# Kernel tuning notes

Measured on AMD Instinct MI355X. Metric: run time of the kernel, lower is better.

## Reference

```python
import jax, jax.numpy as jnp
import numpy as np

B, C, H, W = 8, 64, 256, 256
K = 3  # num_experts in CondConv2D


def setup_inputs() -> dict:
    key = jax.random.key(0)
    ks = jax.random.split(key, 10)
    s = 0.05
    return {
        "x":    jax.random.normal(ks[0], (B, C, H, W), jnp.float32),
        # CondConv2D #1: depthwise 5x5, pad 2, dil 1
        "w0":   jax.random.normal(ks[1], (K, C, 1, 5, 5), jnp.float32) * s,
        "b0":   jax.random.normal(ks[2], (C,), jnp.float32) * s,
        "r0_w": jax.random.normal(ks[3], (K, C), jnp.float32) * s,
        "r0_b": jnp.zeros((K,), jnp.float32),
        # CondConv2D #2: depthwise 7x7, pad 9, dil 3
        "w1":   jax.random.normal(ks[4], (K, C, 1, 7, 7), jnp.float32) * s,
        "b1":   jax.random.normal(ks[5], (C,), jnp.float32) * s,
        "r1_w": jax.random.normal(ks[6], (K, C), jnp.float32) * s,
        "r1_b": jnp.zeros((K,), jnp.float32),
        # conv1: 1x1 pointwise
        "wp":   jax.random.normal(ks[7], (C, C), jnp.float32) * s,
        "bp":   jnp.zeros((C,), jnp.float32),
    }


def cond_dwconv(x, weight, bias, rw, rb, pad, dil):
    """Per-sample expert-mixed depthwise conv (CondConv with groups=C).
    x: [B,C,H,W]; weight: [K,C,1,ks,ks]; rw: [K,C], rb: [K]."""
    b, c, h, w = x.shape
    pooled = x.mean(axis=(2, 3))                      # [B,C] adaptive avg pool to 1x1
    r = jax.nn.sigmoid(pooled @ rw.T + rb)            # [B,K] routing weights
    wk = jnp.einsum('bk,kcihw->bcihw', r, weight)     # [B,C,1,ks,ks] mixed kernels
    ksz = weight.shape[-1]
    # batch-folded grouped conv: fold B into channel/group dim
    out = jax.lax.conv_general_dilated(
        x.reshape(1, b * c, h, w),
        wk.reshape(b * c, 1, ksz, ksz),
        window_strides=(1, 1),
        padding=[(pad, pad), (pad, pad)],
        rhs_dilation=(dil, dil),
        feature_group_count=b * c,
        dimension_numbers=('NCHW', 'OIHW', 'NCHW'))
    return out.reshape(b, c, h, w) + bias[None, :, None, None]


def reference(x, w0, b0, r0_w, r0_b, w1, b1, r1_w, r1_b, wp, bp):
    attn = jax.nn.gelu(cond_dwconv(x, w0, b0, r0_w, r0_b, pad=2, dil=1), approximate=False)
    attn = jax.nn.gelu(cond_dwconv(attn, w1, b1, r1_w, r1_b, pad=9, dil=3), approximate=False)
    attn = jnp.einsum('bchw,oc->bohw', attn, wp) + bp[None, :, None, None]  # 1x1 conv
    return x * attn
```

## Files before the change

kernel.cpp:

```cpp
#include <hip/hip_runtime.h>
#include <hip/hip_fp16.h>

#define HW 65536
#define PW 256
#define C7S 168

__device__ __forceinline__ float gelu_f(float v) {
    return 0.5f * v * (1.0f + erff(v * 0.7071067811865476f));
}

__device__ __forceinline__ unsigned pack2h(float a, float b) {
    __half2 h = __floats2half2_rn(a, b);
    return *reinterpret_cast<unsigned*>(&h);
}

__device__ __forceinline__ void unpack8(uint4 u, float* dst) {
    float2 f;
    f = __half22float2(*reinterpret_cast<__half2*>(&u.x)); dst[0] = f.x; dst[1] = f.y;
    f = __half22float2(*reinterpret_cast<__half2*>(&u.y)); dst[2] = f.x; dst[3] = f.y;
    f = __half22float2(*reinterpret_cast<__half2*>(&u.z)); dst[4] = f.x; dst[5] = f.y;
    f = __half22float2(*reinterpret_cast<__half2*>(&u.w)); dst[6] = f.x; dst[7] = f.y;
}

__device__ __forceinline__ float sgpr_f(float v) {
    union { float f; int i; } u;
    u.f = v;
    u.i = __builtin_amdgcn_readfirstlane(u.i);
    return u.f;
}

__global__ __launch_bounds__(256) void k_pool_x(const float* __restrict__ x,
                                                float* __restrict__ partial) {
    __shared__ float red[256];
    const int t = threadIdx.x;
    const int blk = blockIdx.x;
    const float* p = x + (size_t)blk * 16384;
    float s = 0.f;
    #pragma unroll
    for (int i = 0; i < 16; ++i) {
        float4 v = *reinterpret_cast<const float4*>(p + (i * 256 + t) * 4);
        s += v.x + v.y + v.z + v.w;
    }
    red[t] = s;
    __syncthreads();
    for (int off = 128; off > 0; off >>= 1) {
        if (t < off) red[t] += red[t + off];
        __syncthreads();
    }
    if (t == 0) partial[blk] = red[0];
}

__global__ __launch_bounds__(64) void k_route_mix(const float* __restrict__ partial,
                                                  const float* __restrict__ rw,
                                                  const float* __restrict__ rb,
                                                  const float* __restrict__ wexp,
                                                  float* __restrict__ wkout, int taps) {
    __shared__ float pool_s[64];
    __shared__ float r_s[3];
    const int b = blockIdx.x, c = threadIdx.x;
    float s = 0.f;
    #pragma unroll
    for (int q = 0; q < 4; ++q) s += partial[(b * 64 + c) * 4 + q];
    pool_s[c] = s * (1.0f / 65536.0f);
    __syncthreads();
    if (c < 3) {
        float z = rb[c];
        #pragma unroll
        for (int i = 0; i < 64; ++i) z += pool_s[i] * rw[c * 64 + i];
        r_s[c] = 1.0f / (1.0f + expf(-z));
    }
    __syncthreads();
    const float r0 = r_s[0], r1 = r_s[1], r2 = r_s[2];
    for (int j = 0; j < taps; ++j) {
        wkout[(b * 64 + c) * taps + j] =
            r0 * wexp[(0 * 64 + c) * taps + j] +
            r1 * wexp[(1 * 64 + c) * taps + j] +
            r2 * wexp[(2 * 64 + c) * taps + j];
    }
}

__global__ __launch_bounds__(256) void k_conv5(const float* __restrict__ x,
                                               const float* __restrict__ wk,
                                               const float* __restrict__ bias,
                                               __half* __restrict__ attn0,
                                               float* __restrict__ tilesum) {
    __shared__ float red[256];
    const int blk = blockIdx.x;
    const int plane = blk >> 2;
    const int tile = blk & 3;
    const int c = plane & 63;
    const int oy0 = (tile >> 1) << 7;
    const int ox0 = (tile & 1) << 7;
    const int t = threadIdx.x;
    const int ox = ox0 + ((t & 15) << 3);
    const int oy = oy0 + ((t >> 4) << 3);
    const float* xp = x + (size_t)plane * HW;
    const float* wkp = wk + plane * 25;
    float w[25];
    #pragma unroll
    for (int i = 0; i < 25; ++i) w[i] = sgpr_f(wkp[i]);
    float acc[8][8];
    #pragma unroll
    for (int i = 0; i < 8; ++i)
        #pragma unroll
        for (int j = 0; j < 8; ++j) acc[i][j] = 0.f;

    #pragma unroll
    for (int r = 0; r < 12; ++r) {
        const int gy = oy - 2 + r;
        if (gy >= 0 && gy < 256) {
            const float* rp = xp + gy * PW + ox;
            float buf[16];
            float4 v;
            if (ox > 0) v = *reinterpret_cast<const float4*>(rp - 4);
            else        v = make_float4(0.f, 0.f, 0.f, 0.f);
            buf[0] = v.x; buf[1] = v.y; buf[2] = v.z; buf[3] = v.w;
            v = *reinterpret_cast<const float4*>(rp);
            buf[4] = v.x; buf[5] = v.y; buf[6] = v.z; buf[7] = v.w;
            v = *reinterpret_cast<const float4*>(rp + 4);
            buf[8] = v.x; buf[9] = v.y; buf[10] = v.z; buf[11] = v.w;
            if (ox < 248) v = *reinterpret_cast<const float4*>(rp + 8);
            else          v = make_float4(0.f, 0.f, 0.f, 0.f);
            buf[12] = v.x; buf[13] = v.y; buf[14] = v.z; buf[15] = v.w;
            #pragma unroll
            for (int i = 0; i < 8; ++i) {
                const int d = r - i;
                if (d >= 0 && d <= 4) {
                    #pragma unroll
                    for (int dx = 0; dx < 5; ++dx) {
                        const float wv = w[d * 5 + dx];
                        #pragma unroll
                        for (int j = 0; j < 8; ++j)
                            acc[i][j] += wv * buf[j + dx + 2];
                    }
                }
            }
        }
    }
    const float bs = bias[c];
    float lsum = 0.f;
    __half* op = attn0 + (size_t)plane * HW;
    #pragma unroll
    for (int i = 0; i < 8; ++i) {
        float g[8];
        #pragma unroll
        for (int j = 0; j < 8; ++j) {
            g[j] = gelu_f(acc[i][j] + bs);
            lsum += g[j];
        }
        uint4 st;
        st.x = pack2h(g[0], g[1]); st.y = pack2h(g[2], g[3]);
        st.z = pack2h(g[4], g[5]); st.w = pack2h(g[6], g[7]);
        *reinterpret_cast<uint4*>(op + (oy + i) * PW + ox) = st;
    }
    red[t] = lsum;
    __syncthreads();
    for (int off = 128; off > 0; off >>= 1) {
        if (t < off) red[t] += red[t + off];
        __syncthreads();
    }
    if (t == 0) tilesum[blk] = red[0];
}

__global__ __launch_bounds__(256) void k_conv7(const __half* __restrict__ a0,
                                               const float* __restrict__ wk,
                                               const float* __restrict__ bias,
                                               __half* __restrict__ attn1) {
    __shared__ __half lds[82 * C7S];
    const int blk = blockIdx.x;
    const int plane = blk >> 3;
    const int tile = blk & 7;
    const int c = plane & 63;
    const int oy0 = (tile >> 1) << 6;
    const int ox0 = (tile & 1) << 7;
    const int t = threadIdx.x;
    const __half* ap = a0 + (size_t)plane * HW;

    const uint4 z4 = make_uint4(0u, 0u, 0u, 0u);
    #pragma unroll
    for (int it = 0; it < 7; ++it) {
        const int idx = it * 256 + t;
        if (idx < 1722) {
            const int lr = idx / 21;
            const int c8 = idx - lr * 21;
            const int gy = oy0 - 9 + lr;
            const int gx = ox0 - 16 + (c8 << 3);
            uint4 v = z4;
            if ((unsigned)gy < 256u && (unsigned)gx < 256u)
                v = *reinterpret_cast<const uint4*>(ap + gy * PW + gx);
            *reinterpret_cast<uint4*>(&lds[lr * C7S + (c8 << 3)]) = v;
        }
    }

    float w[49];
    #pragma unroll
    for (int i = 0; i < 49; ++i) w[i] = sgpr_f(wk[plane * 49 + i]);
    __syncthreads();

    const int tx = t & 3, ty = t >> 2;
    const int ox = tx << 5;
    float acc[32];
    #pragma unroll
    for (int j = 0; j < 32; ++j) acc[j] = 0.f;

    #pragma unroll
    for (int dyi = 0; dyi < 7; ++dyi) {
        const int lr = ty + 3 * dyi;
        const __half* lp = &lds[lr * C7S + ox];
        float buf[64];
        #pragma unroll
        for (int k = 0; k < 8; ++k) {
            uint4 u = *reinterpret_cast<const uint4*>(lp + (k << 3));
            unpack8(u, buf + (k << 3));
        }
        #pragma unroll
        for (int dxi = 0; dxi < 7; ++dxi) {
            const float wv = w[dyi * 7 + dxi];
            #pragma unroll
            for (int j = 0; j < 32; ++j)
                acc[j] += wv * buf[7 + j + 3 * dxi];
        }
    }

    const float bs = bias[c];
    __half* op = attn1 + (size_t)plane * HW + (size_t)(oy0 + ty) * PW + ox0 + ox;
    #pragma unroll
    for (int q = 0; q < 4; ++q) {
        float g[8];
        #pragma unroll
        for (int j = 0; j < 8; ++j) g[j] = gelu_f(acc[q * 8 + j] + bs);
        uint4 st;
        st.x = pack2h(g[0], g[1]); st.y = pack2h(g[2], g[3]);
        st.z = pack2h(g[4], g[5]); st.w = pack2h(g[6], g[7]);
        *reinterpret_cast<uint4*>(op + (q << 3)) = st;
    }
}

__global__ __launch_bounds__(256) void k_mix(const __half* __restrict__ attn1,
                                             const float* __restrict__ wpm,
                                             const float* __restrict__ bp,
                                             const float* __restrict__ x,
                                             float* __restrict__ out) {
    __shared__ __half A_s[64][256];
    __shared__ float wpT[64][64];
    const int t = threadIdx.x;
    const int blk = blockIdx.x;
    const int b = blk >> 8;
    const int p0g = (blk & 255) << 8;
    #pragma unroll
    for (int it = 0; it < 8; ++it) {
        const int ci = it * 256 + t;
        const int row = ci >> 5;
        const int off = (ci & 31) << 3;
        uint4 u = *reinterpret_cast<const uint4*>(attn1 + (size_t)(b * 64 + row) * HW + p0g + off);
        *reinterpret_cast<uint4*>(&A_s[row][off]) = u;
    }
    #pragma unroll
    for (int j = 0; j < 16; ++j) {
        const int idx = j * 256 + t;
        const int cc = idx & 63;
        const int oo = idx >> 6;
        wpT[cc][oo] = wpm[oo * 64 + cc];
    }
    __syncthreads();
    const int o0 = (t >> 5) << 3;
    const int p0 = (t & 31) << 3;
    float acc[8][8];
    #pragma unroll
    for (int i = 0; i < 8; ++i)
        #pragma unroll
        for (int j = 0; j < 8; ++j) acc[i][j] = 0.f;
    #pragma unroll 4
    for (int cc = 0; cc < 64; ++cc) {
        float4 wa = *reinterpret_cast<const float4*>(&wpT[cc][o0]);
        float4 wb = *reinterpret_cast<const float4*>(&wpT[cc][o0 + 4]);
        const float wv[8] = {wa.x, wa.y, wa.z, wa.w, wb.x, wb.y, wb.z, wb.w};
        float af[8];
        uint4 u = *reinterpret_cast<const uint4*>(&A_s[cc][p0]);
        unpack8(u, af);
        #pragma unroll
        for (int oo = 0; oo < 8; ++oo) {
            const float wvv = wv[oo];
            #pragma unroll
            for (int pp = 0; pp < 8; ++pp) acc[oo][pp] += wvv * af[pp];
        }
    }
    #pragma unroll
    for (int oo = 0; oo < 8; ++oo) {
        const int o = o0 + oo;
        const float bb = bp[o];
        const size_t base = (size_t)(b * 64 + o) * HW + p0g + p0;
        float4 x0 = *reinterpret_cast<const float4*>(x + base);
        float4 x1 = *reinterpret_cast<const float4*>(x + base + 4);
        float4 r0, r1;
        r0.x = x0.x * (acc[oo][0] + bb); r0.y = x0.y * (acc[oo][1] + bb);
        r0.z = x0.z * (acc[oo][2] + bb); r0.w = x0.w * (acc[oo][3] + bb);
        r1.x = x1.x * (acc[oo][4] + bb); r1.y = x1.y * (acc[oo][5] + bb);
        r1.z = x1.z * (acc[oo][6] + bb); r1.w = x1.w * (acc[oo][7] + bb);
        *reinterpret_cast<float4*>(out + base) = r0;
        *reinterpret_cast<float4*>(out + base + 4) = r1;
    }
}

extern "C" void kernel_launch(void* const* d_in, const int* in_sizes, int n_in,
                              void* d_out, int out_size, void* d_ws, size_t ws_size,
                              hipStream_t stream) {
    const float* x   = (const float*)d_in[0];
    const float* w0  = (const float*)d_in[1];
    const float* b0  = (const float*)d_in[2];
    const float* r0w = (const float*)d_in[3];
    const float* r0b = (const float*)d_in[4];
    const float* w1  = (const float*)d_in[5];
    const float* b1  = (const float*)d_in[6];
    const float* r1w = (const float*)d_in[7];
    const float* r1b = (const float*)d_in[8];
    const float* wpm = (const float*)d_in[9];
    const float* bp  = (const float*)d_in[10];
    float* out = (float*)d_out;

    char* ws = (char*)d_ws;
    __half* attn0   = (__half*)(ws);
    __half* attn1   = (__half*)(ws + 67108864);
    float* partial0 = (float*)(ws + 134217728);
    float* tilesum1 = (float*)(ws + 134217728 + 8192);
    float* wk0      = (float*)(ws + 134217728 + 16384);
    float* wk1      = (float*)(ws + 134217728 + 16384 + 51200);

    k_pool_x<<<2048, 256, 0, stream>>>(x, partial0);
    k_route_mix<<<8, 64, 0, stream>>>(partial0, r0w, r0b, w0, wk0, 25);
    k_conv5<<<2048, 256, 0, stream>>>(x, wk0, b0, attn0, tilesum1);
    k_route_mix<<<8, 64, 0, stream>>>(tilesum1, r1w, r1b, w1, wk1, 49);
    k_conv7<<<4096, 256, 0, stream>>>(attn0, wk1, b1, attn1);
    k_mix<<<2048, 256, 0, stream>>>(attn1, wpm, bp, x, out);
}
```

Baseline: 271.8 us.

## Stage conv5 input tile in LDS and compute 1x32 row strips per thread

The 5x5 depthwise conv now stages a 68x136 halo tile of the input plane in shared memory, loaded with coalesced float4 reads. Previously each thread read overlapping rows straight from global memory. Each thread now computes a 1x32 horizontal strip from LDS rows instead of an 8x8 block, and tiles shrink to 64x128, so the grid doubles to 4096 blocks. The routing kernel takes a partial-count parameter to handle 8 tile sums per plane, and workspace offsets are adjusted to fit. In exchange, the kernel uses more shared memory and needs an extra barrier, and halo rows are loaded redundantly across the smaller tiles.

```diff
diff --git a/kernel.cpp b/kernel.cpp
--- a/kernel.cpp
+++ b/kernel.cpp
@@ -4,6 +4,7 @@
 #define HW 65536
 #define PW 256
 #define C7S 168
+#define C5S 140
 
 __device__ __forceinline__ float gelu_f(float v) {
     return 0.5f * v * (1.0f + erff(v * 0.7071067811865476f));
@@ -54,13 +55,13 @@
                                                   const float* __restrict__ rw,
                                                   const float* __restrict__ rb,
                                                   const float* __restrict__ wexp,
-                                                  float* __restrict__ wkout, int taps) {
+                                                  float* __restrict__ wkout,
+                                                  int taps, int parts) {
     __shared__ float pool_s[64];
     __shared__ float r_s[3];
     const int b = blockIdx.x, c = threadIdx.x;
     float s = 0.f;
-    #pragma unroll
-    for (int q = 0; q < 4; ++q) s += partial[(b * 64 + c) * 4 + q];
+    for (int q = 0; q < parts; ++q) s += partial[(b * 64 + c) * parts + q];
     pool_s[c] = s * (1.0f / 65536.0f);
     __syncthreads();
     if (c < 3) {
@@ -84,74 +85,78 @@
                                                const float* __restrict__ bias,
                                                __half* __restrict__ attn0,
                                                float* __restrict__ tilesum) {
+    __shared__ float lds[68 * C5S];
     __shared__ float red[256];
     const int blk = blockIdx.x;
-    const int plane = blk >> 2;
-    const int tile = blk & 3;
+    const int plane = blk >> 3;
+    const int tile = blk & 7;
     const int c = plane & 63;
-    const int oy0 = (tile >> 1) << 7;
+    const int oy0 = (tile >> 1) << 6;
     const int ox0 = (tile & 1) << 7;
     const int t = threadIdx.x;
-    const int ox = ox0 + ((t & 15) << 3);
-    const int oy = oy0 + ((t >> 4) << 3);
     const float* xp = x + (size_t)plane * HW;
-    const float* wkp = wk + plane * 25;
+
+    #pragma unroll
+    for (int it = 0; it < 10; ++it) {
+        const int idx = it * 256 + t;
+        if (idx < 2312) {
+            const int lr = idx / 34;
+            const int c4 = idx - lr * 34;
+            const int gy = oy0 - 2 + lr;
+            const int gx = ox0 - 4 + (c4 << 2);
+            float4 v = make_float4(0.f, 0.f, 0.f, 0.f);
+            if ((unsigned)gy < 256u && (unsigned)gx < 256u)
+                v = *reinterpret_cast<const float4*>(xp + gy * PW + gx);
+            *reinterpret_cast<float4*>(&lds[lr * C5S + (c4 << 2)]) = v;
+        }
+    }
+
     float w[25];
     #pragma unroll
-    for (int i = 0; i < 25; ++i) w[i] = sgpr_f(wkp[i]);
-    float acc[8][8];
-    #pragma unroll
-    for (int i = 0; i < 8; ++i)
-        #pragma unroll
-        for (int j = 0; j < 8; ++j) acc[i][j] = 0.f;
-
-    #pragma unroll
-    for (int r = 0; r < 12; ++r) {
-        const int gy = oy - 2 + r;
-        if (gy >= 0 && gy < 256) {
-            const float* rp = xp + gy * PW + ox;
-            float buf[16];
-            float4 v;
-            if (ox > 0) v = *reinterpret_cast<const float4*>(rp - 4);
-            else        v = make_float4(0.f, 0.f, 0.f, 0.f);
-            buf[0] = v.x; buf[1] = v.y; buf[2] = v.z; buf[3] = v.w;
-            v = *reinterpret_cast<const float4*>(rp);
-            buf[4] = v.x; buf[5] = v.y; buf[6] = v.z; buf[7] = v.w;
-            v = *reinterpret_cast<const float4*>(rp + 4);
-            buf[8] = v.x; buf[9] = v.y; buf[10] = v.z; buf[11] = v.w;
-            if (ox < 248) v = *reinterpret_cast<const float4*>(rp + 8);
-            else          v = make_float4(0.f, 0.f, 0.f, 0.f);
-            buf[12] = v.x; buf[13] = v.y; buf[14] = v.z; buf[15] = v.w;
+    for (int i = 0; i < 25; ++i) w[i] = sgpr_f(wk[plane * 25 + i]);
+    __syncthreads();
+
+    const int tx = t & 3, ty = t >> 2;
+    const int ox = tx << 5;
+    float acc[32];
+    #pragma unroll
+    for (int j = 0; j < 32; ++j) acc[j] = 0.f;
+
+    #pragma unroll
+    for (int dy = 0; dy < 5; ++dy) {
+        const int lr = ty + dy;
+        const float* lp = &lds[lr * C5S + ox];
+        float buf[40];
+        #pragma unroll
+        for (int k = 0; k < 10; ++k) {
+            float4 v = *reinterpret_cast<const float4*>(lp + (k << 2));
+            buf[k * 4 + 0] = v.x; buf[k * 4 + 1] = v.y;
+            buf[k * 4 + 2] = v.z; buf[k * 4 + 3] = v.w;
+        }
+        #pragma unroll
+        for (int dx = 0; dx < 5; ++dx) {
+            const float wv = w[dy * 5 + dx];
             #pragma unroll
-            for (int i = 0; i < 8; ++i) {
-                const int d = r - i;
-                if (d >= 0 && d <= 4) {
-                    #pragma unroll
-                    for (int dx = 0; dx < 5; ++dx) {
-                        const float wv = w[d * 5 + dx];
-                        #pragma unroll
-                        for (int j = 0; j < 8; ++j)
-                            acc[i][j] += wv * buf[j + dx + 2];
-                    }
-                }
-            }
-        }
-    }
+            for (int j = 0; j < 32; ++j)
+                acc[j] += wv * buf[j + dx + 2];
+        }
+    }
+
     const float bs = bias[c];
     float lsum = 0.f;
-    __half* op = attn0 + (size_t)plane * HW;
-    #pragma unroll
-    for (int i = 0; i < 8; ++i) {
+    __half* op = attn0 + (size_t)plane * HW + (size_t)(oy0 + ty) * PW + ox0 + ox;
+    #pragma unroll
+    for (int q = 0; q < 4; ++q) {
         float g[8];
         #pragma unroll
         for (int j = 0; j < 8; ++j) {
-            g[j] = gelu_f(acc[i][j] + bs);
+            g[j] = gelu_f(acc[q * 8 + j] + bs);
             lsum += g[j];
         }
         uint4 st;
         st.x = pack2h(g[0], g[1]); st.y = pack2h(g[2], g[3]);
         st.z = pack2h(g[4], g[5]); st.w = pack2h(g[6], g[7]);
-        *reinterpret_cast<uint4*>(op + (oy + i) * PW + ox) = st;
+        *reinterpret_cast<uint4*>(op + (q << 3)) = st;
     }
     red[t] = lsum;
     __syncthreads();
@@ -322,14 +327,14 @@
     __half* attn0   = (__half*)(ws);
     __half* attn1   = (__half*)(ws + 67108864);
     float* partial0 = (float*)(ws + 134217728);
-    float* tilesum1 = (float*)(ws + 134217728 + 8192);
-    float* wk0      = (float*)(ws + 134217728 + 16384);
-    float* wk1      = (float*)(ws + 134217728 + 16384 + 51200);
+    float* tilesum1 = (float*)(ws + 134217728 + 16384);
+    float* wk0      = (float*)(ws + 134217728 + 65536);
+    float* wk1      = (float*)(ws + 134217728 + 65536 + 51200);
 
     k_pool_x<<<2048, 256, 0, stream>>>(x, partial0);
-    k_route_mix<<<8, 64, 0, stream>>>(partial0, r0w, r0b, w0, wk0, 25);
-    k_conv5<<<2048, 256, 0, stream>>>(x, wk0, b0, attn0, tilesum1);
-    k_route_mix<<<8, 64, 0, stream>>>(tilesum1, r1w, r1b, w1, wk1, 49);
+    k_route_mix<<<8, 64, 0, stream>>>(partial0, r0w, r0b, w0, wk0, 25, 4);
+    k_conv5<<<4096, 256, 0, stream>>>(x, wk0, b0, attn0, tilesum1);
+    k_route_mix<<<8, 64, 0, stream>>>(tilesum1, r1w, r1b, w1, wk1, 49, 8);
     k_conv7<<<4096, 256, 0, stream>>>(attn0, wk1, b1, attn1);
     k_mix<<<2048, 256, 0, stream>>>(attn1, wpm, bp, x, out);
 }
```

Result: slower. 318.7 us (+17.3%).
